# Performance work log

Hardware: AMD Instinct MI355X
Metric: run time of the kernel (lower is better)

## Reference

```python
import jax, jax.numpy as jnp
import numpy as np

CELL = 128
STEPS = 20
N_KEYS = 4   # ['first_conn','second_conn','first_op','second_op']
N_OUT = 6


def setup_inputs() -> dict:
    key = jax.random.key(0)
    ks = jax.random.split(key, 10)
    s = 0.05
    return {
        "net": jax.random.randint(ks[0], (STEPS,), 0, N_OUT),          # sampled actions, each in [0,6)
        "reward": jax.random.uniform(ks[1], (1,), dtype=jnp.float32),   # unused in forward (kept for signature parity)
        "emb_start": jax.random.normal(ks[2], (1, CELL), jnp.float32) * s,          # Embedding(1,128)
        "emb_keys": jax.random.normal(ks[3], (N_KEYS, N_OUT, CELL), jnp.float32) * s,
        "fc_W": jax.random.normal(ks[4], (N_KEYS, N_OUT, CELL), jnp.float32) * s,
        "fc_b": jax.random.normal(ks[5], (N_KEYS, N_OUT), jnp.float32) * s,
        "W_ih": jax.random.normal(ks[6], (4 * CELL, CELL), jnp.float32) * s,  # LSTMCell input weights (i,f,g,o)
        "W_hh": jax.random.normal(ks[7], (4 * CELL, CELL), jnp.float32) * s,  # LSTMCell hidden weights
        "b_ih": jax.random.normal(ks[8], (4 * CELL,), jnp.float32) * s,
        "b_hh": jax.random.normal(ks[9], (4 * CELL,), jnp.float32) * s,
    }


def _lstm_cell(x, h, c, W_ih, W_hh, b_ih, b_hh):
    # PyTorch LSTMCell: gates ordered (i, f, g, o)
    gates = x @ W_ih.T + b_ih + h @ W_hh.T + b_hh   # [1, 4*CELL]
    i, f, g, o = jnp.split(gates, 4, axis=-1)
    c_new = jax.nn.sigmoid(f) * c + jax.nn.sigmoid(i) * jnp.tanh(g)
    h_new = jax.nn.sigmoid(o) * jnp.tanh(c_new)
    return h_new, c_new


def reference(net, reward, emb_start, emb_keys, fc_W, fc_b, W_ih, W_hh, b_ih, b_hh):
    key_idx = jnp.arange(STEPS) % N_KEYS            # which head/embedding at each step
    fc_W_t = fc_W[key_idx]                          # [STEPS, 6, CELL]
    fc_b_t = fc_b[key_idx]                          # [STEPS, 6]
    emb_t = emb_keys[key_idx, net]                  # [STEPS, CELL] next-step input embedding

    def step(carry, xs):
        h, c, x = carry
        Wt, bt, ev = xs
        h, c = _lstm_cell(x, h, c, W_ih, W_hh, b_ih, b_hh)
        probs = jax.nn.softmax(h @ Wt.T + bt, axis=1)   # [1, 6]
        return (h, c, ev[None, :]), probs

    h0 = jnp.zeros((1, CELL), dtype=emb_start.dtype)
    c0 = jnp.zeros((1, CELL), dtype=emb_start.dtype)
    x0 = emb_start                                   # embedding lookup of action 0 in a 1-row table
    _, outputs = jax.lax.scan(step, (h0, c0, x0), (fc_W_t, fc_b_t, emb_t))
    return outputs                                   # [STEPS, 1, 6], stacked version of the torch list
```

## Files before the change

kernel.cpp:

```cpp
#include <hip/hip_runtime.h>
#include <hip/hip_fp16.h>

#define CELL 128
#define STEPS 20

typedef _Float16 half8_t __attribute__((ext_vector_type(8)));
typedef float    floatx4 __attribute__((ext_vector_type(4)));

__device__ __forceinline__ unsigned packf2(float x, float y) {
    typedef _Float16 h2 __attribute__((ext_vector_type(2)));
    h2 h = { (_Float16)x, (_Float16)y };
    return __builtin_bit_cast(unsigned, h);
}
__device__ __forceinline__ float fdot2u(unsigned a, unsigned b, float c) {
    typedef _Float16 h2 __attribute__((ext_vector_type(2)));
#if __has_builtin(__builtin_amdgcn_fdot2)
    return __builtin_amdgcn_fdot2(__builtin_bit_cast(h2, a), __builtin_bit_cast(h2, b), c, false);
#else
    h2 x = __builtin_bit_cast(h2, a), y = __builtin_bit_cast(h2, b);
    return fmaf((float)x[0], (float)y[0], fmaf((float)x[1], (float)y[1], c));
#endif
}
__device__ __forceinline__ float fast_sigmoid(float x) { return 1.0f / (1.0f + __expf(-x)); }
__device__ __forceinline__ float fast_tanh(float x) {
    return 2.0f / (1.0f + __expf(-2.0f * x)) - 1.0f;
}
__device__ __forceinline__ half8_t cvt8(const float* p) {
    const float4* p4 = (const float4*)p;
    float4 a = p4[0], b = p4[1];
    return half8_t{ (_Float16)a.x, (_Float16)a.y, (_Float16)a.z, (_Float16)a.w,
                    (_Float16)b.x, (_Float16)b.y, (_Float16)b.z, (_Float16)b.w };
}

extern "C" __global__ void __launch_bounds__(512, 1)
nas_policy_kernel(const int* __restrict__ net,
                  const float* __restrict__ emb_start,
                  const float* __restrict__ emb_keys,
                  const float* __restrict__ fc_W,
                  const float* __restrict__ fc_b,
                  const float* __restrict__ W_ih,
                  const float* __restrict__ W_hh,
                  const float* __restrict__ b_ih,
                  const float* __restrict__ b_hh,
                  float* __restrict__ out)
{
    const int t0   = threadIdx.x;
    const int wv   = t0 >> 6;
    const int lane = t0 & 63;
    const int quad = lane >> 4;
    const int lcol = lane & 15;

    __shared__ __align__(16) unsigned s_xv2[32 * 68];
    __shared__ __align__(16) float    s_gx[STEPS * 512];
    __shared__ __align__(16) unsigned hbuf[2 * 64];
    __shared__ unsigned s_fcw2[24 * 64];
    __shared__ float    s_fcb[24];
    __shared__ float    llog[STEPS * 8];

    for (int i = t0; i < STEPS * 64; i += 512) {
        const int m = i >> 6, j = i & 63;
        const float2* src = (m == 0) ? (const float2*)emb_start
            : (const float2*)(emb_keys + ((((m - 1) & 3) * 6) + net[m - 1]) * CELL);
        float2 v = src[j];
        s_xv2[m * 68 + j] = packf2(v.x, v.y);
    }
    {
        const float2* fw2 = (const float2*)fc_W;
        for (int i = t0; i < 24 * 64; i += 512) { float2 w = fw2[i]; s_fcw2[i] = packf2(w.x, w.y); }
    }
    if (t0 < 24) s_fcb[t0] = fc_b[t0];
    if (t0 < 64) hbuf[64 + t0] = 0u;

    const int rr0 = (wv << 4) + lcol;
    float biasx[4];
#pragma unroll
    for (int tau = 0; tau < 4; ++tau) {
        const int r = tau * 128 + rr0;
        biasx[tau] = b_ih[r] + b_hh[r];
    }

    __syncthreads();

    {
        half8_t bw[4][4];
#pragma unroll
        for (int kc = 0; kc < 4; ++kc) {
            const int k0 = kc * 32 + quad * 8;
#pragma unroll
            for (int tau = 0; tau < 4; ++tau)
                bw[kc][tau] = cvt8(W_ih + (tau * 128 + rr0) * CELL + k0);
        }
        floatx4 ax0[4] = { {0,0,0,0}, {0,0,0,0}, {0,0,0,0}, {0,0,0,0} };
        floatx4 ax1[4] = { {0,0,0,0}, {0,0,0,0}, {0,0,0,0}, {0,0,0,0} };
#pragma unroll
        for (int kc = 0; kc < 4; ++kc) {
            uint4 u0 = *(const uint4*)&s_xv2[lcol * 68 + kc * 16 + quad * 4];
            uint4 u1 = *(const uint4*)&s_xv2[(16 + lcol) * 68 + kc * 16 + quad * 4];
            half8_t a0f = __builtin_bit_cast(half8_t, u0);
            half8_t a1f = __builtin_bit_cast(half8_t, u1);
#pragma unroll
            for (int tau = 0; tau < 4; ++tau) {
                ax0[tau] = __builtin_amdgcn_mfma_f32_16x16x32_f16(a0f, bw[kc][tau], ax0[tau], 0, 0, 0);
                ax1[tau] = __builtin_amdgcn_mfma_f32_16x16x32_f16(a1f, bw[kc][tau], ax1[tau], 0, 0, 0);
            }
        }
#pragma unroll
        for (int tau = 0; tau < 4; ++tau) {
            const int r = tau * 128 + rr0;
#pragma unroll
            for (int reg = 0; reg < 4; ++reg)
                s_gx[(quad * 4 + reg) * 512 + r] = ax0[tau][reg] + biasx[tau];
            if (quad == 0) {
#pragma unroll
                for (int reg = 0; reg < 4; ++reg)
                    s_gx[(16 + reg) * 512 + r] = ax1[tau][reg] + biasx[tau];
            }
        }
    }
    __builtin_amdgcn_sched_barrier(0);

    half8_t bf0[4], bf1[4], bf2[4], bf3[4];
#pragma unroll
    for (int kc = 0; kc < 4; ++kc) {
        const int k0 = kc * 32 + quad * 8;
        bf0[kc] = cvt8(W_hh + (0 * 128 + rr0) * CELL + k0);
        bf1[kc] = cvt8(W_hh + (1 * 128 + rr0) * CELL + k0);
        bf2[kc] = cvt8(W_hh + (2 * 128 + rr0) * CELL + k0);
        bf3[kc] = cvt8(W_hh + (3 * 128 + rr0) * CELL + k0);
    }

    float c = 0.0f;
    __syncthreads();

    for (int t = 0; t < STEPS; ++t) {
        const uint4* hp4 = (const uint4*)(hbuf + (((t + 1) & 1) << 6));
        floatx4 a0 = {0,0,0,0}, a1 = {0,0,0,0}, a2 = {0,0,0,0}, a3 = {0,0,0,0};
#pragma unroll
        for (int kc = 0; kc < 4; ++kc) {
            uint4 u = hp4[(kc << 2) + quad];
            half8_t af = __builtin_bit_cast(half8_t, u);
            a0 = __builtin_amdgcn_mfma_f32_16x16x32_f16(af, bf0[kc], a0, 0, 0, 0);
            a1 = __builtin_amdgcn_mfma_f32_16x16x32_f16(af, bf1[kc], a1, 0, 0, 0);
            a2 = __builtin_amdgcn_mfma_f32_16x16x32_f16(af, bf2[kc], a2, 0, 0, 0);
            a3 = __builtin_amdgcn_mfma_f32_16x16x32_f16(af, bf3[kc], a3, 0, 0, 0);
        }

        if (t >= 1 && wv >= 6 && lane >= 16) {
            const int hd = (wv - 6) * 3 + (lane >> 4) - 1;
            const int li = lane & 15;
            const int hg = ((t - 1) & 3) * 6 + hd;
            const unsigned* hb = hbuf + (((t + 1) & 1) << 6);
            const unsigned* wp = s_fcw2 + hg * 64 + li * 4;
            float p = fdot2u(hb[li * 4],     wp[0], 0.0f);
            p = fdot2u(hb[li * 4 + 1], wp[1], p);
            p = fdot2u(hb[li * 4 + 2], wp[2], p);
            p = fdot2u(hb[li * 4 + 3], wp[3], p);
            p += __shfl_down(p, 8); p += __shfl_down(p, 4);
            p += __shfl_down(p, 2); p += __shfl_down(p, 1);
            if (li == 0) llog[(t - 1) * 8 + hd] = p + s_fcb[hg];
        }

        if (lane < 16) {
            const int base = t * 512 + (wv << 4) + lane;
            float ig = fast_sigmoid(a0[0] + s_gx[base]);
            float fg = fast_sigmoid(a1[0] + s_gx[base + 128]);
            float gg = fast_tanh   (a2[0] + s_gx[base + 256]);
            float og = fast_sigmoid(a3[0] + s_gx[base + 384]);
            c = fg * c + ig * gg;
            float h = og * fast_tanh(c);
            float hpv = __shfl_xor(h, 1);
            if ((lane & 1) == 0)
                hbuf[((t & 1) << 6) + (wv << 3) + (lane >> 1)] = packf2(h, hpv);
        }

        __syncthreads();
    }

    if (wv >= 6 && lane >= 16) {
        const int hd = (wv - 6) * 3 + (lane >> 4) - 1;
        const int li = lane & 15;
        const int hg = (19 & 3) * 6 + hd;
        const unsigned* hb = hbuf + 64;
        const unsigned* wp = s_fcw2 + hg * 64 + li * 4;
        float p = fdot2u(hb[li * 4],     wp[0], 0.0f);
        p = fdot2u(hb[li * 4 + 1], wp[1], p);
        p = fdot2u(hb[li * 4 + 2], wp[2], p);
        p = fdot2u(hb[li * 4 + 3], wp[3], p);
        p += __shfl_down(p, 8); p += __shfl_down(p, 4);
        p += __shfl_down(p, 2); p += __shfl_down(p, 1);
        if (li == 0) llog[19 * 8 + hd] = p + s_fcb[hg];
    }
    __syncthreads();
    if (t0 < STEPS * 6) {
        const int s = t0 / 6, k = t0 - s * 6;
        const float* L = llog + s * 8;
        float l0 = L[0], l1 = L[1], l2 = L[2], l3 = L[3], l4 = L[4], l5 = L[5];
        float m = fmaxf(fmaxf(fmaxf(l0, l1), fmaxf(l2, l3)), fmaxf(l4, l5));
        float e0 = __expf(l0 - m), e1 = __expf(l1 - m), e2 = __expf(l2 - m);
        float e3 = __expf(l3 - m), e4 = __expf(l4 - m), e5 = __expf(l5 - m);
        float sum = ((e0 + e1) + (e2 + e3)) + (e4 + e5);
        float mine = (k == 0) ? e0 : (k == 1) ? e1 : (k == 2) ? e2
                   : (k == 3) ? e3 : (k == 4) ? e4 : e5;
        out[t0] = mine / sum;
    }
}

extern "C" void kernel_launch(void* const* d_in, const int* in_sizes, int n_in,
                              void* d_out, int out_size, void* d_ws, size_t ws_size,
                              hipStream_t stream) {
    (void)in_sizes; (void)n_in; (void)out_size; (void)d_ws; (void)ws_size;
    const int*   net       = (const int*)d_in[0];
    const float* emb_start = (const float*)d_in[2];
    const float* emb_keys  = (const float*)d_in[3];
    const float* fc_W      = (const float*)d_in[4];
    const float* fc_b      = (const float*)d_in[5];
    const float* W_ih      = (const float*)d_in[6];
    const float* W_hh      = (const float*)d_in[7];
    const float* b_ih      = (const float*)d_in[8];
    const float* b_hh      = (const float*)d_in[9];
    float*       out       = (float*)d_out;

    hipLaunchKernelGGL(nas_policy_kernel, dim3(1), dim3(512), 0, stream,
                       net, emb_start, emb_keys, fc_W, fc_b,
                       W_ih, W_hh, b_ih, b_hh, out);
}
```

Before: 105.6 us.

## Spread LSTM gate activations across quads and split MFMA accumulation chains

```diff
diff --git a/kernel.cpp b/kernel.cpp
--- a/kernel.cpp
+++ b/kernel.cpp
@@ -21,9 +21,12 @@
     return fmaf((float)x[0], (float)y[0], fmaf((float)x[1], (float)y[1], c));
 #endif
 }
-__device__ __forceinline__ float fast_sigmoid(float x) { return 1.0f / (1.0f + __expf(-x)); }
-__device__ __forceinline__ float fast_tanh(float x) {
-    return 2.0f / (1.0f + __expf(-2.0f * x)) - 1.0f;
+__device__ __forceinline__ float fastrcp(float x) {
+#if __has_builtin(__builtin_amdgcn_rcpf)
+    return __builtin_amdgcn_rcpf(x);
+#else
+    return 1.0f / x;
+#endif
 }
 __device__ __forceinline__ half8_t cvt8(const float* p) {
     const float4* p4 = (const float4*)p;
@@ -117,7 +120,6 @@
             }
         }
     }
-    __builtin_amdgcn_sched_barrier(0);
 
     half8_t bf0[4], bf1[4], bf2[4], bf3[4];
 #pragma unroll
@@ -129,26 +131,43 @@
         bf3[kc] = cvt8(W_hh + (3 * 128 + rr0) * CELL + k0);
     }
 
+    const float ascale = (quad == 2) ? 2.0f : 1.0f;
+    const float amul   = (quad == 2) ? 2.0f : 1.0f;
+    const float aadd   = (quad == 2) ? -1.0f : 0.0f;
+
     float c = 0.0f;
     __syncthreads();
 
     for (int t = 0; t < STEPS; ++t) {
         const uint4* hp4 = (const uint4*)(hbuf + (((t + 1) & 1) << 6));
-        floatx4 a0 = {0,0,0,0}, a1 = {0,0,0,0}, a2 = {0,0,0,0}, a3 = {0,0,0,0};
-#pragma unroll
-        for (int kc = 0; kc < 4; ++kc) {
-            uint4 u = hp4[(kc << 2) + quad];
-            half8_t af = __builtin_bit_cast(half8_t, u);
-            a0 = __builtin_amdgcn_mfma_f32_16x16x32_f16(af, bf0[kc], a0, 0, 0, 0);
-            a1 = __builtin_amdgcn_mfma_f32_16x16x32_f16(af, bf1[kc], a1, 0, 0, 0);
-            a2 = __builtin_amdgcn_mfma_f32_16x16x32_f16(af, bf2[kc], a2, 0, 0, 0);
-            a3 = __builtin_amdgcn_mfma_f32_16x16x32_f16(af, bf3[kc], a3, 0, 0, 0);
-        }
-
-        if (t >= 1 && wv >= 6 && lane >= 16) {
-            const int hd = (wv - 6) * 3 + (lane >> 4) - 1;
+        floatx4 a0a = {0,0,0,0}, a0b = {0,0,0,0}, a1a = {0,0,0,0}, a1b = {0,0,0,0};
+        floatx4 a2a = {0,0,0,0}, a2b = {0,0,0,0}, a3a = {0,0,0,0}, a3b = {0,0,0,0};
+        {
+            uint4 u0 = hp4[(0 << 2) + quad], u1 = hp4[(1 << 2) + quad];
+            uint4 u2 = hp4[(2 << 2) + quad], u3 = hp4[(3 << 2) + quad];
+            half8_t f0 = __builtin_bit_cast(half8_t, u0), f1 = __builtin_bit_cast(half8_t, u1);
+            half8_t f2 = __builtin_bit_cast(half8_t, u2), f3 = __builtin_bit_cast(half8_t, u3);
+            a0a = __builtin_amdgcn_mfma_f32_16x16x32_f16(f0, bf0[0], a0a, 0, 0, 0);
+            a1a = __builtin_amdgcn_mfma_f32_16x16x32_f16(f0, bf1[0], a1a, 0, 0, 0);
+            a2a = __builtin_amdgcn_mfma_f32_16x16x32_f16(f0, bf2[0], a2a, 0, 0, 0);
+            a3a = __builtin_amdgcn_mfma_f32_16x16x32_f16(f0, bf3[0], a3a, 0, 0, 0);
+            a0b = __builtin_amdgcn_mfma_f32_16x16x32_f16(f1, bf0[1], a0b, 0, 0, 0);
+            a1b = __builtin_amdgcn_mfma_f32_16x16x32_f16(f1, bf1[1], a1b, 0, 0, 0);
+            a2b = __builtin_amdgcn_mfma_f32_16x16x32_f16(f1, bf2[1], a2b, 0, 0, 0);
+            a3b = __builtin_amdgcn_mfma_f32_16x16x32_f16(f1, bf3[1], a3b, 0, 0, 0);
+            a0a = __builtin_amdgcn_mfma_f32_16x16x32_f16(f2, bf0[2], a0a, 0, 0, 0);
+            a1a = __builtin_amdgcn_mfma_f32_16x16x32_f16(f2, bf1[2], a1a, 0, 0, 0);
+            a2a = __builtin_amdgcn_mfma_f32_16x16x32_f16(f2, bf2[2], a2a, 0, 0, 0);
+            a3a = __builtin_amdgcn_mfma_f32_16x16x32_f16(f2, bf3[2], a3a, 0, 0, 0);
+            a0b = __builtin_amdgcn_mfma_f32_16x16x32_f16(f3, bf0[3], a0b, 0, 0, 0);
+            a1b = __builtin_amdgcn_mfma_f32_16x16x32_f16(f3, bf1[3], a1b, 0, 0, 0);
+            a2b = __builtin_amdgcn_mfma_f32_16x16x32_f16(f3, bf2[3], a2b, 0, 0, 0);
+            a3b = __builtin_amdgcn_mfma_f32_16x16x32_f16(f3, bf3[3], a3b, 0, 0, 0);
+        }
+
+        if (t >= 1 && wv < 6 && quad == 1) {
             const int li = lane & 15;
-            const int hg = ((t - 1) & 3) * 6 + hd;
+            const int hg = ((t - 1) & 3) * 6 + wv;
             const unsigned* hb = hbuf + (((t + 1) & 1) << 6);
             const unsigned* wp = s_fcw2 + hg * 64 + li * 4;
             float p = fdot2u(hb[li * 4],     wp[0], 0.0f);
@@ -157,17 +176,23 @@
             p = fdot2u(hb[li * 4 + 3], wp[3], p);
             p += __shfl_down(p, 8); p += __shfl_down(p, 4);
             p += __shfl_down(p, 2); p += __shfl_down(p, 1);
-            if (li == 0) llog[(t - 1) * 8 + hd] = p + s_fcb[hg];
-        }
-
+            if (li == 0) llog[(t - 1) * 8 + wv] = p + s_fcb[hg];
+        }
+
+        float gsum = (quad == 0) ? (a0a[0] + a0b[0])
+                   : (quad == 1) ? (a1a[0] + a1b[0])
+                   : (quad == 2) ? (a2a[0] + a2b[0])
+                   :               (a3a[0] + a3b[0]);
+        float u = gsum + s_gx[t * 512 + quad * 128 + rr0];
+        float act = fmaf(amul, fastrcp(1.0f + __expf(-ascale * u)), aadd);
+
+        float fg = __shfl(act, lane + 16);
+        float gg = __shfl(act, lane + 32);
+        float og = __shfl(act, lane + 48);
         if (lane < 16) {
-            const int base = t * 512 + (wv << 4) + lane;
-            float ig = fast_sigmoid(a0[0] + s_gx[base]);
-            float fg = fast_sigmoid(a1[0] + s_gx[base + 128]);
-            float gg = fast_tanh   (a2[0] + s_gx[base + 256]);
-            float og = fast_sigmoid(a3[0] + s_gx[base + 384]);
-            c = fg * c + ig * gg;
-            float h = og * fast_tanh(c);
+            c = fg * c + act * gg;
+            float th = fmaf(2.0f, fastrcp(1.0f + __expf(-2.0f * c)), -1.0f);
+            float h = og * th;
             float hpv = __shfl_xor(h, 1);
             if ((lane & 1) == 0)
                 hbuf[((t & 1) << 6) + (wv << 3) + (lane >> 1)] = packf2(h, hpv);
@@ -176,10 +201,9 @@
         __syncthreads();
     }
 
-    if (wv >= 6 && lane >= 16) {
-        const int hd = (wv - 6) * 3 + (lane >> 4) - 1;
+    if (wv < 6 && quad == 1) {
         const int li = lane & 15;
-        const int hg = (19 & 3) * 6 + hd;
+        const int hg = (19 & 3) * 6 + wv;
         const unsigned* hb = hbuf + 64;
         const unsigned* wp = s_fcw2 + hg * 64 + li * 4;
         float p = fdot2u(hb[li * 4],     wp[0], 0.0f);
@@ -188,7 +212,7 @@
         p = fdot2u(hb[li * 4 + 3], wp[3], p);
         p += __shfl_down(p, 8); p += __shfl_down(p, 4);
         p += __shfl_down(p, 2); p += __shfl_down(p, 1);
-        if (li == 0) llog[19 * 8 + hd] = p + s_fcb[hg];
+        if (li == 0) llog[19 * 8 + wv] = p + s_fcb[hg];
     }
     __syncthreads();
     if (t0 < STEPS * 6) {
```

After: 99.40 us. 1.06x faster.
